# Kernel optimization log

Hardware: AMD Instinct MI355X
Metric: run time of the kernel (lower is better)

The kernel has to match this reference:

```python
import math
import jax, jax.numpy as jnp
import numpy as np

B, LQ, LK, D_IN, D_HID, D_VAL = 32, 2048, 50, 1024, 1024, 512
MASK_VALUE = -1000000.0  # original uses -1e6, not -inf


def setup_inputs() -> dict:
    key = jax.random.key(0)
    ks = jax.random.split(key, 8)
    s = 1.0 / math.sqrt(D_IN)
    return {
        "queries": jax.random.normal(ks[0], (B, LQ, D_IN), dtype=jnp.float32),
        "keys": jax.random.normal(ks[1], (B, LK, D_IN), dtype=jnp.float32),
        "values": jax.random.normal(ks[2], (B, LQ, D_IN), dtype=jnp.float32),
        "valid_lens": jax.random.randint(ks[3], (B,), 0, LQ),
        "W_q": jax.random.normal(ks[4], (D_IN, D_HID), dtype=jnp.float32) * s,
        "W_k": jax.random.normal(ks[5], (D_IN, D_HID), dtype=jnp.float32) * s,
        "W_v": jax.random.normal(ks[6], (D_IN, D_HID), dtype=jnp.float32) * s,
        "W_o": jax.random.normal(ks[7], (LK, D_VAL), dtype=jnp.float32) * (1.0 / math.sqrt(LK)),
    }


def reference(queries, keys, values, valid_lens, W_q, W_k, W_v, W_o):
    q = jnp.einsum("bqi,ih->bqh", queries, W_q)          # [B, Lq, H]
    k = jnp.einsum("bki,ih->bkh", keys, W_k)             # [B, Lk, H]
    d = q.shape[-1]
    scores = jnp.einsum("bqh,bkh->bqk", q, k) / math.sqrt(d)   # [B, Lq, Lk]
    scores = jnp.einsum("bqk,kv->bvq", scores, W_o)            # w_o linear + permute -> [B, V, Lq]
    # mask along last (query) axis: positions >= valid_len get -1e6
    mask = jnp.arange(LQ)[None, None, :] < valid_lens[:, None, None]   # [B, 1, Lq]
    scores = jnp.where(mask, scores, MASK_VALUE)
    attn = jax.nn.softmax(scores, axis=-1)                     # [B, V, Lq]
    v = jnp.einsum("bqi,ih->bqh", values, W_v)                 # [B, Lq, H]
    out = jnp.einsum("bvq,bqh->bvh", attn, v)                  # [B, V, H]
    return out, attn
```

## Files before the change

kernel.cpp:

```cpp
#include <hip/hip_runtime.h>
#include <hip/hip_bf16.h>


#define NB   32
#define LQ   2048
#define LK   50
#define DIN  1024
#define DHID 1024
#define DVAL 512

typedef short bf16x8 __attribute__((ext_vector_type(8)));
typedef float f32x4  __attribute__((ext_vector_type(4)));
typedef unsigned short u16x8 __attribute__((ext_vector_type(8)));
typedef unsigned short u16x4 __attribute__((ext_vector_type(4)));

static __device__ __forceinline__ unsigned short f2b(float f) {
  __hip_bfloat16 h = __float2bfloat16(f);
  unsigned short u;
  __builtin_memcpy(&u, &h, 2);
  return u;
}

static __device__ __forceinline__ void gload_lds16(const void* g, void* l) {
  __builtin_amdgcn_global_load_lds(
      (const __attribute__((address_space(1))) void*)g,
      (__attribute__((address_space(3))) void*)l, 16, 0, 0);
}

__global__ __launch_bounds__(256) void cvt_bf16_kernel(
    const float* __restrict__ in, unsigned short* __restrict__ outp, long n) {
  const long i = ((long)blockIdx.x * 256 + threadIdx.x) * 8;
  if (i >= n) return;
  const float4 a = *reinterpret_cast<const float4*>(in + i);
  const float4 b = *reinterpret_cast<const float4*>(in + i + 4);
  u16x8 p;
  p[0] = f2b(a.x); p[1] = f2b(a.y); p[2] = f2b(a.z); p[3] = f2b(a.w);
  p[4] = f2b(b.x); p[5] = f2b(b.y); p[6] = f2b(b.z); p[7] = f2b(b.w);
  *reinterpret_cast<u16x8*>(outp + i) = p;
}

__global__ __launch_bounds__(256) void transpose_bf16_kernel(
    const float* __restrict__ in, unsigned short* __restrict__ outp,
    int R, int C, long sIn, long sOut) {
  __shared__ float t[64][65];
  in   += (long)blockIdx.z * sIn;
  outp += (long)blockIdx.z * sOut;
  const int r0 = blockIdx.y * 64, c0 = blockIdx.x * 64;
  const int tid = threadIdx.x;
  const int lr = tid >> 4;
  const int lc = (tid & 15) * 4;
#pragma unroll
  for (int u = 0; u < 4; ++u) {
    const float4 v = *reinterpret_cast<const float4*>(
        in + (long)(r0 + lr + u * 16) * C + c0 + lc);
    t[lc + 0][lr + u * 16] = v.x; t[lc + 1][lr + u * 16] = v.y;
    t[lc + 2][lr + u * 16] = v.z; t[lc + 3][lr + u * 16] = v.w;
  }
  __syncthreads();
  const int orow = tid >> 2;
  const int oseg = (tid & 3) * 16;
  u16x8 p0, p1;
#pragma unroll
  for (int u = 0; u < 8; ++u) p0[u] = f2b(t[orow][oseg + u]);
#pragma unroll
  for (int u = 0; u < 8; ++u) p1[u] = f2b(t[orow][oseg + 8 + u]);
  unsigned short* o = outp + (long)(c0 + orow) * R + r0 + oseg;
  *reinterpret_cast<u16x8*>(o)     = p0;
  *reinterpret_cast<u16x8*>(o + 8) = p1;
}

__global__ __launch_bounds__(256) void kb_kernel(
    const float* __restrict__ keys, unsigned short* __restrict__ kb) {
  const int row = blockIdx.x;
  const int b = row >> 7, r = row & 127;
  const int t = threadIdx.x;
  u16x4 o;
  if (r < LK) {
    const float4 v = *reinterpret_cast<const float4*>(
        keys + ((long)b * LK + r) * DIN + t * 4);
    o[0] = f2b(v.x); o[1] = f2b(v.y); o[2] = f2b(v.z); o[3] = f2b(v.w);
  } else {
    o[0] = 0; o[1] = 0; o[2] = 0; o[3] = 0;
  }
  *reinterpret_cast<u16x4*>(kb + (long)row * DIN + t * 4) = o;
}

#define VB 8
__global__ __launch_bounds__(256) void nb_kernel(
    const float* __restrict__ P, const float* __restrict__ W_o,
    unsigned short* __restrict__ Nb) {
  const int blk = blockIdx.x;
  const int b  = blk / (DVAL / VB);
  const int v0 = (blk % (DVAL / VB)) * VB;
  const int t  = threadIdx.x;
  const float* Pb = P + (long)b * 128 * DHID + t * 4;
  f32x4 acc[VB];
#pragma unroll
  for (int u = 0; u < VB; ++u) acc[u] = (f32x4)(0.0f);
  for (int k = 0; k < LK; ++k) {
    const f32x4 pv = *reinterpret_cast<const f32x4*>(Pb + (long)k * DHID);
#pragma unroll
    for (int u = 0; u < VB; ++u) {
      const float wo = W_o[k * DVAL + v0 + u];
      acc[u] += pv * wo;
    }
  }
#pragma unroll
  for (int u = 0; u < VB; ++u) {
    u16x4 r;
    r[0] = f2b(acc[u][0] * 0.03125f); r[1] = f2b(acc[u][1] * 0.03125f);
    r[2] = f2b(acc[u][2] * 0.03125f); r[3] = f2b(acc[u][3] * 0.03125f);
    *reinterpret_cast<u16x4*>(
        Nb + ((long)b * DVAL + v0 + u) * DHID + t * 4) = r;
  }
}

#define BM 128
#define BN 128
#define BK 64

template <typename OT>
__global__ __launch_bounds__(256, 3) void gemm_bt_kernel(
    const unsigned short* __restrict__ Ag, const unsigned short* __restrict__ Bg,
    OT* __restrict__ Cg, int K, int lda, int ldb, int ldc,
    long sA, long sB, long sC) {
  __shared__ __attribute__((aligned(16))) unsigned short As[BM * BK];
  __shared__ __attribute__((aligned(16))) unsigned short Bs[BN * BK];

  const int tid = threadIdx.x;

  const int gx  = gridDim.x, gy = gridDim.y;
  const int gxy = gx * gy;
  const int nwg = gxy * gridDim.z;
  const int lin = (blockIdx.z * gy + blockIdx.y) * gx + blockIdx.x;
  const int swz = (lin & 7) * (nwg >> 3) + (lin >> 3);
  const int bz  = swz / gxy;
  const int rem = swz - bz * gxy;
  const int bx  = rem / gy;
  const int by  = rem - bx * gy;

  Ag += (long)bz * sA;
  Bg += (long)bz * sB;
  Cg += (long)bz * sC;
  const int m0 = by * BM;
  const int n0 = bx * BN;

  const int w    = tid >> 6;
  const int lane = tid & 63;
  const int l15  = lane & 15;
  const int quad = lane >> 4;
  const int wm   = (w >> 1) * 64;
  const int wn   = (w & 1) * 64;

  const int srow = w * 8 + (lane >> 3);
  const int scol = (lane & 7) * 8;
  const unsigned short* aptr = Ag + (long)(m0 + srow) * lda + scol;
  const unsigned short* bptr = Bg + (long)(n0 + srow) * ldb + scol;
  unsigned short* adst = &As[srow * BK + scol];
  unsigned short* bdst = &Bs[srow * BK + scol];

  f32x4 acc[4][4];
#pragma unroll
  for (int i = 0; i < 4; ++i)
#pragma unroll
    for (int j = 0; j < 4; ++j) acc[i][j] = (f32x4)(0.0f);

  for (int k0 = 0; k0 < K; k0 += BK) {
#pragma unroll
    for (int r = 0; r < 4; ++r)
      gload_lds16(aptr + (long)(r * 32) * lda + k0, adst + r * 32 * BK);
#pragma unroll
    for (int r = 0; r < 4; ++r)
      gload_lds16(bptr + (long)(r * 32) * ldb + k0, bdst + r * 32 * BK);
    __syncthreads();

#pragma unroll
    for (int ks = 0; ks < BK; ks += 32) {
      bf16x8 af[4], bfv[4];
#pragma unroll
      for (int i = 0; i < 4; ++i)
        af[i] = *reinterpret_cast<const bf16x8*>(
            &As[(wm + i * 16 + l15) * BK + ks + quad * 8]);
#pragma unroll
      for (int j = 0; j < 4; ++j)
        bfv[j] = *reinterpret_cast<const bf16x8*>(
            &Bs[(wn + j * 16 + l15) * BK + ks + quad * 8]);
#pragma unroll
      for (int i = 0; i < 4; ++i)
#pragma unroll
        for (int j = 0; j < 4; ++j)
          acc[i][j] = __builtin_amdgcn_mfma_f32_16x16x32_bf16(
              af[i], bfv[j], acc[i][j], 0, 0, 0);
    }
    __syncthreads();
  }

#pragma unroll
  for (int i = 0; i < 4; ++i) {
#pragma unroll
    for (int j = 0; j < 4; ++j) {
#pragma unroll
      for (int r = 0; r < 4; ++r) {
        const int row = m0 + wm + i * 16 + quad * 4 + r;
        const int col = n0 + wn + j * 16 + l15;
        const float val = acc[i][j][r];
        if constexpr (sizeof(OT) == 2) {
          reinterpret_cast<__hip_bfloat16*>(Cg)[(long)row * ldc + col] =
              __float2bfloat16(val);
        } else {
          reinterpret_cast<float*>(Cg)[(long)row * ldc + col] = val;
        }
      }
    }
  }
}

__global__ __launch_bounds__(256) void softmax_kernel(
    float* __restrict__ attn, unsigned short* __restrict__ attnb,
    const int* __restrict__ vlens) {
  __shared__ float smax[4], ssum[4];
  const long base = (long)blockIdx.x * LQ;
  const int vl = vlens[blockIdx.x >> 9];
  const int t = threadIdx.x;
  float x[8];
  float mx = -3.0e38f;
#pragma unroll
  for (int u = 0; u < 8; ++u) {
    const int q = u * 256 + t;
    float v = attn[base + q];
    if (q >= vl) v = -1000000.0f;
    x[u] = v;
    mx = fmaxf(mx, v);
  }
#pragma unroll
  for (int off = 32; off > 0; off >>= 1) mx = fmaxf(mx, __shfl_down(mx, off));
  if ((t & 63) == 0) smax[t >> 6] = mx;
  __syncthreads();
  mx = fmaxf(fmaxf(smax[0], smax[1]), fmaxf(smax[2], smax[3]));
  float s = 0.f;
#pragma unroll
  for (int u = 0; u < 8; ++u) { x[u] = __expf(x[u] - mx); s += x[u]; }
#pragma unroll
  for (int off = 32; off > 0; off >>= 1) s += __shfl_down(s, off);
  if ((t & 63) == 0) ssum[t >> 6] = s;
  __syncthreads();
  s = ssum[0] + ssum[1] + ssum[2] + ssum[3];
  const float inv = 1.0f / s;
#pragma unroll
  for (int u = 0; u < 8; ++u) {
    const float v = x[u] * inv;
    attn[base + u * 256 + t] = v;
    attnb[base + u * 256 + t] = f2b(v);
  }
}

extern "C" void kernel_launch(void* const* d_in, const int* in_sizes, int n_in,
                              void* d_out, int out_size, void* d_ws, size_t ws_size,
                              hipStream_t stream) {
  const float* queries = (const float*)d_in[0];
  const float* keys    = (const float*)d_in[1];
  const float* values  = (const float*)d_in[2];
  const int*   vlens   = (const int*)d_in[3];
  const float* W_q     = (const float*)d_in[4];
  const float* W_k     = (const float*)d_in[5];
  const float* W_v     = (const float*)d_in[6];
  const float* W_o     = (const float*)d_in[7];

  float* out  = (float*)d_out;
  float* attn = out + (size_t)NB * DVAL * DHID;

  char* ws = (char*)d_ws;
  unsigned short* qb    = (unsigned short*)(ws + 0);
  unsigned short* vT    = qb;
  unsigned short* kb    = (unsigned short*)(ws + 134217728UL);
  float*          Pb    = (float*)(ws + 142606336UL);
  unsigned short* Gt    = (unsigned short*)(ws + 159383552UL);
  unsigned short* wkb   = (unsigned short*)(ws + 161480704UL);
  unsigned short* attnb = (unsigned short*)(ws + 134217728UL);
  unsigned short* Nb    = (unsigned short*)(ws + 201326592UL);
  unsigned short* Tb    = Nb;
  unsigned short* wqb   = (unsigned short*)(ws + 234881024UL);
  unsigned short* wvT   = (unsigned short*)(ws + 236978176UL);

  cvt_bf16_kernel<<<dim3(32768), 256, 0, stream>>>(queries, qb, (long)NB * LQ * DIN);
  cvt_bf16_kernel<<<dim3(512),   256, 0, stream>>>(W_q, wqb, (long)DIN * DHID);
  cvt_bf16_kernel<<<dim3(512),   256, 0, stream>>>(W_k, wkb, (long)DIN * DHID);
  transpose_bf16_kernel<<<dim3(16, 16, 1), 256, 0, stream>>>(W_v, wvT, DIN, DHID, 0, 0);
  kb_kernel<<<dim3(NB * 128), 256, 0, stream>>>(keys, kb);

  gemm_bt_kernel<__hip_bfloat16><<<dim3(8, 8, 1), 256, 0, stream>>>(
      wqb, wkb, (__hip_bfloat16*)Gt, 1024, 1024, 1024, 1024, 0, 0, 0);

  gemm_bt_kernel<float><<<dim3(8, 1, NB), 256, 0, stream>>>(
      kb, Gt, Pb, 1024, 1024, 1024, 1024,
      (long)128 * 1024, 0, (long)128 * 1024);

  nb_kernel<<<dim3(NB * (DVAL / VB)), 256, 0, stream>>>(Pb, W_o, Nb);

  gemm_bt_kernel<float><<<dim3(16, 4, NB), 256, 0, stream>>>(
      Nb, qb, attn, 1024, 1024, 1024, 2048,
      (long)512 * 1024, (long)2048 * 1024, (long)512 * 2048);

  transpose_bf16_kernel<<<dim3(16, 32, NB), 256, 0, stream>>>(
      values, vT, LQ, DIN, (long)LQ * DIN, (long)DIN * LQ);

  softmax_kernel<<<dim3(NB * DVAL), 256, 0, stream>>>(attn, attnb, vlens);

  gemm_bt_kernel<__hip_bfloat16><<<dim3(8, 4, NB), 256, 0, stream>>>(
      attnb, vT, (__hip_bfloat16*)Tb, 2048, 2048, 2048, 1024,
      (long)512 * 2048, (long)1024 * 2048, (long)512 * 1024);

  gemm_bt_kernel<float><<<dim3(8, 4, NB), 256, 0, stream>>>(
      Tb, wvT, out, 1024, 1024, 1024, 1024,
      (long)512 * 1024, 0, (long)512 * 1024);
}
```

Baseline: 1.035 ms.

## Double-buffer GEMM LDS tiles with XOR swizzle and prefetch two tiles ahead

The bf16 GEMM kernel now holds two LDS buffers per operand. It prefetches the tile two steps ahead with global_load_lds while computing on the current one, and uses explicit vmcnt waits and barriers in place of syncthreads. Global source columns are XOR-swizzled per row so LDS reads avoid bank conflicts, and MFMA blocks run at raised wave priority. LDS use doubles, so occupancy drops from 3 to 2 workgroups per CU.

```diff
diff --git a/kernel.cpp b/kernel.cpp
--- a/kernel.cpp
+++ b/kernel.cpp
@@ -120,12 +120,12 @@
 #define BK 64
 
 template <typename OT>
-__global__ __launch_bounds__(256, 3) void gemm_bt_kernel(
+__global__ __launch_bounds__(256, 2) void gemm_bt_kernel(
     const unsigned short* __restrict__ Ag, const unsigned short* __restrict__ Bg,
     OT* __restrict__ Cg, int K, int lda, int ldb, int ldc,
     long sA, long sB, long sC) {
-  __shared__ __attribute__((aligned(16))) unsigned short As[BM * BK];
-  __shared__ __attribute__((aligned(16))) unsigned short Bs[BN * BK];
+  __shared__ __attribute__((aligned(16))) unsigned short As[2][BM * BK];
+  __shared__ __attribute__((aligned(16))) unsigned short Bs[2][BN * BK];
 
   const int tid = threadIdx.x;
 
@@ -152,12 +152,11 @@
   const int wm   = (w >> 1) * 64;
   const int wn   = (w & 1) * 64;
 
-  const int srow = w * 8 + (lane >> 3);
-  const int scol = (lane & 7) * 8;
-  const unsigned short* aptr = Ag + (long)(m0 + srow) * lda + scol;
-  const unsigned short* bptr = Bg + (long)(n0 + srow) * ldb + scol;
-  unsigned short* adst = &As[srow * BK + scol];
-  unsigned short* bdst = &Bs[srow * BK + scol];
+  const int srow  = w * 8 + (lane >> 3);
+  const int sldsc = (lane & 7) * 8;
+  const int sglbc = ((lane & 7) ^ (lane >> 3)) * 8;
+  const unsigned short* aptr = Ag + (long)(m0 + srow) * lda + sglbc;
+  const unsigned short* bptr = Bg + (long)(n0 + srow) * ldb + sglbc;
 
   f32x4 acc[4][4];
 #pragma unroll
@@ -165,34 +164,62 @@
 #pragma unroll
     for (int j = 0; j < 4; ++j) acc[i][j] = (f32x4)(0.0f);
 
-  for (int k0 = 0; k0 < K; k0 += BK) {
-#pragma unroll
-    for (int r = 0; r < 4; ++r)
-      gload_lds16(aptr + (long)(r * 32) * lda + k0, adst + r * 32 * BK);
-#pragma unroll
-    for (int r = 0; r < 4; ++r)
-      gload_lds16(bptr + (long)(r * 32) * ldb + k0, bdst + r * 32 * BK);
-    __syncthreads();
-
+  const int nt = K >> 6;
+
+#pragma unroll
+  for (int tt = 0; tt < 2; ++tt) {
+#pragma unroll
+    for (int r = 0; r < 4; ++r) {
+      gload_lds16(aptr + (long)(r * 32) * lda + tt * BK,
+                  &As[tt][(srow + r * 32) * BK + sldsc]);
+      gload_lds16(bptr + (long)(r * 32) * ldb + tt * BK,
+                  &Bs[tt][(srow + r * 32) * BK + sldsc]);
+    }
+  }
+  asm volatile("s_waitcnt vmcnt(8)" ::: "memory");
+  asm volatile("s_barrier" ::: "memory");
+
+  for (int t = 0; t < nt; ++t) {
+    const int cur = t & 1;
 #pragma unroll
     for (int ks = 0; ks < BK; ks += 32) {
       bf16x8 af[4], bfv[4];
 #pragma unroll
-      for (int i = 0; i < 4; ++i)
+      for (int i = 0; i < 4; ++i) {
+        const int row = wm + i * 16 + l15;
         af[i] = *reinterpret_cast<const bf16x8*>(
-            &As[(wm + i * 16 + l15) * BK + ks + quad * 8]);
-#pragma unroll
-      for (int j = 0; j < 4; ++j)
+            &As[cur][(row * BK + ks + quad * 8) ^ ((row & 7) << 3)]);
+      }
+#pragma unroll
+      for (int j = 0; j < 4; ++j) {
+        const int row = wn + j * 16 + l15;
         bfv[j] = *reinterpret_cast<const bf16x8*>(
-            &Bs[(wn + j * 16 + l15) * BK + ks + quad * 8]);
+            &Bs[cur][(row * BK + ks + quad * 8) ^ ((row & 7) << 3)]);
+      }
+      __builtin_amdgcn_s_setprio(1);
 #pragma unroll
       for (int i = 0; i < 4; ++i)
 #pragma unroll
         for (int j = 0; j < 4; ++j)
           acc[i][j] = __builtin_amdgcn_mfma_f32_16x16x32_bf16(
               af[i], bfv[j], acc[i][j], 0, 0, 0);
-    }
-    __syncthreads();
+      __builtin_amdgcn_s_setprio(0);
+    }
+    asm volatile("s_barrier" ::: "memory");
+    if (t + 2 < nt) {
+      const long k0 = (long)(t + 2) * BK;
+#pragma unroll
+      for (int r = 0; r < 4; ++r) {
+        gload_lds16(aptr + (long)(r * 32) * lda + k0,
+                    &As[cur][(srow + r * 32) * BK + sldsc]);
+        gload_lds16(bptr + (long)(r * 32) * ldb + k0,
+                    &Bs[cur][(srow + r * 32) * BK + sldsc]);
+      }
+      asm volatile("s_waitcnt vmcnt(8)" ::: "memory");
+    } else {
+      asm volatile("s_waitcnt vmcnt(0)" ::: "memory");
+    }
+    asm volatile("s_barrier" ::: "memory");
   }
 
 #pragma unroll
```

After: 1.001 ms. 1.03x faster.
